# Kernel optimization log

Hardware: AMD Instinct MI355X
Metric: run time of the kernel (lower is better)

Reference implementation:

```python
import jax, jax.numpy as jnp
import numpy as np

TOP_K = 2
NUM_EXPERTS = 64
SEQ, BS, HS = 2048, 4, 4096
TOKENS = SEQ * BS  # tokens_per_batch
TOL = 1e-4
EPS = 1e-8


def sinkhorn(temp_cost):
    # temp_cost: (T, E) float32 logits. Mirrors SinkhornRouter.sinkhorn exactly.
    cost = jnp.exp(temp_cost)
    n0, n1 = cost.shape
    # initial d0 (overwritten inside loop in torch too, kept for fidelity of carry dtype/shape)
    d0 = (TOKENS / NUM_EXPERTS) * jnp.sum(jnp.exp(2.0 * temp_cost), axis=1)
    d1 = jnp.ones((n1,), dtype=cost.dtype)
    err0 = jnp.asarray(1e9, dtype=cost.dtype)

    def cond(carry):
        _, _, err = carry
        return err > TOL

    def body(carry):
        d0, d1, _ = carry  # d1 here plays the role of d1_old
        d0_new = (1.0 / n0) / (jnp.sum(d1 * cost, axis=1) + EPS)          # (T,)
        d1_new = (1.0 / n1) / (jnp.sum(d0_new[:, None] * cost, axis=0) + EPS)  # (E,)
        err = jnp.mean(jnp.abs(d1 - d1_new))
        return (d0_new, d1_new, err)

    d0, d1, _ = jax.lax.while_loop(cond, body, (d0, d1, err0))
    return d1 * cost * d0[:, None]


def setup_inputs() -> dict:
    key = jax.random.key(0)
    kx, kw = jax.random.split(key)
    x = jax.random.normal(kx, (SEQ, BS, HS), dtype=jnp.float32)
    W = jax.random.normal(kw, (NUM_EXPERTS, HS), dtype=jnp.float32) * 0.02
    return {"x": x, "W": W}


def reference(x, W):
    # router logits: (T, E)
    logits = jnp.reshape(x, (-1, x.shape[-1])) @ W.T
    # Sinkhorn normalization is done in fp32 under no_grad in torch -> stop_gradient
    norm_logits = sinkhorn(jax.lax.stop_gradient(logits).astype(jnp.float32))
    _, indices = jax.lax.top_k(norm_logits, TOP_K)  # (T, top_k) int32
    # top_k > 1 -> softmax activation (fp32, cast back)
    probs = jax.nn.softmax(logits.astype(jnp.float32), axis=-1).astype(logits.dtype)
    scores = jnp.take_along_axis(probs, indices, axis=1)  # (T, top_k)
    return scores, indices
```

## Files before the change

kernel.cpp:

```cpp
#include <hip/hip_runtime.h>
#include <hip/hip_cooperative_groups.h>
#include <math.h>

namespace cg = cooperative_groups;

namespace {
constexpr int kTokens = 8192;
constexpr int kHS = 4096;
constexpr float kTol = 1e-4f;
constexpr float kEps = 1e-8f;
constexpr int kMaxIters = 1000;
constexpr int kSinkBlocks = 64;
constexpr size_t kTagFloats = 128;
constexpr size_t kGdataFloats = 2 * 64 * 64;
constexpr size_t kLogitsOff = kTagFloats + kGdataFloats;
constexpr size_t kLogitsFloats = (size_t)kTokens * 64;
constexpr size_t kWtpFloats = (size_t)(kHS / 4) * 64 * 4;
}

__device__ __forceinline__ float wave_sum(float v) {
#pragma unroll
  for (int o = 32; o; o >>= 1) v += __shfl_xor(v, o, 64);
  return v;
}

typedef __attribute__((ext_vector_type(8))) short bf16x8;
typedef __attribute__((ext_vector_type(4))) float f32x4;

__device__ __forceinline__ unsigned short f2bf(float x) {
  unsigned u = __builtin_bit_cast(unsigned, x);
  u += 0x7fffu + ((u >> 16) & 1u);
  return (unsigned short)(u >> 16);
}

__device__ __forceinline__ void split8(const float* p, bf16x8& hi, bf16x8& lo) {
  const float4 a = *(const float4*)p;
  const float4 b = *(const float4*)(p + 4);
  const float v[8] = {a.x, a.y, a.z, a.w, b.x, b.y, b.z, b.w};
#pragma unroll
  for (int j = 0; j < 8; ++j) {
    const unsigned short h = f2bf(v[j]);
    const float hf = __builtin_bit_cast(float, (unsigned)h << 16);
    hi[j] = (short)h;
    lo[j] = (short)f2bf(v[j] - hf);
  }
}

__global__ void __launch_bounds__(512, 2)
k_logits(const float* __restrict__ X, const float* __restrict__ W,
         float* __restrict__ logits) {
  const int tid = threadIdx.x;
  const int lane = tid & 63;
  const int wid = tid >> 6;
  const int t0 = blockIdx.x * 32;
  const int r = lane & 15;
  const int g = lane >> 4;

  const float* xp = X + (size_t)(t0 + r) * kHS + wid * 512 + g * 8;
  const float* wp = W + (size_t)r * kHS + wid * 512 + g * 8;

  f32x4 acc[2][4];
#pragma unroll
  for (int m = 0; m < 2; ++m)
#pragma unroll
    for (int n = 0; n < 4; ++n) acc[m][n] = (f32x4){0.f, 0.f, 0.f, 0.f};

#pragma unroll 2
  for (int ks = 0; ks < 16; ++ks) {
    const int ko = ks * 32;
    bf16x8 ah[2], al[2], bh[4], bl[4];
#pragma unroll
    for (int m = 0; m < 2; ++m)
      split8(xp + (size_t)(16 * m) * kHS + ko, ah[m], al[m]);
#pragma unroll
    for (int n = 0; n < 4; ++n)
      split8(wp + (size_t)(16 * n) * kHS + ko, bh[n], bl[n]);
#pragma unroll
    for (int m = 0; m < 2; ++m)
#pragma unroll
      for (int n = 0; n < 4; ++n) {
        acc[m][n] = __builtin_amdgcn_mfma_f32_16x16x32_bf16(ah[m], bh[n],
                                                            acc[m][n], 0, 0, 0);
        acc[m][n] = __builtin_amdgcn_mfma_f32_16x16x32_bf16(al[m], bh[n],
                                                            acc[m][n], 0, 0, 0);
        acc[m][n] = __builtin_amdgcn_mfma_f32_16x16x32_bf16(ah[m], bl[n],
                                                            acc[m][n], 0, 0, 0);
      }
  }

  __shared__ __align__(16) float red[8][32][68];
#pragma unroll
  for (int m = 0; m < 2; ++m)
#pragma unroll
    for (int n = 0; n < 4; ++n)
#pragma unroll
      for (int q = 0; q < 4; ++q)
        red[wid][m * 16 + g * 4 + q][n * 16 + r] = acc[m][n][q];
  __syncthreads();

  const int t = tid >> 4;
  const int e4 = (tid & 15) * 4;
  float4 s = *(const float4*)&red[0][t][e4];
#pragma unroll
  for (int w = 1; w < 8; ++w) {
    const float4 p = *(const float4*)&red[w][t][e4];
    s.x += p.x; s.y += p.y; s.z += p.z; s.w += p.w;
  }
  *(float4*)(logits + (size_t)(t0 + t) * 64 + e4) = s;
}

__global__ void __launch_bounds__(1024, 1)
k_sinkhorn(const float* __restrict__ logits, float* __restrict__ out,
           unsigned* __restrict__ tags, float* __restrict__ gdata) {
  const int tid = threadIdx.x;
  const int lane = tid & 63;
  const int wid = __builtin_amdgcn_readfirstlane(tid >> 6);
  const int blk = blockIdx.x;
  __shared__ float lds[1024];

  const int t0 = blk * 128 + wid * 8;
  float lg[8], cst[8];
#pragma unroll
  for (int t = 0; t < 8; ++t) {
    const float a = logits[(size_t)(t0 + t) * 64 + lane];
    lg[t] = a;
    cst[t] = expf(a);
  }

  float d1 = 1.0f;
  float d0v[8];
  int buf = 0;
  for (int it = 0; it < kMaxIters; ++it) {
    float p = 0.0f;
#pragma unroll
    for (int t = 0; t < 8; ++t) {
      const float s = wave_sum(d1 * cst[t]);
      const float d0t = (1.0f / 8192.0f) / (s + kEps);
      d0v[t] = d0t;
      p = fmaf(d0t, cst[t], p);
    }
    __syncthreads();
    lds[wid * 64 + lane] = p;
    __syncthreads();
    const unsigned want = (unsigned)(it + 1);
    if (wid == 0) {
      float bp = 0.0f;
#pragma unroll
      for (int w = 0; w < 16; ++w) bp += lds[w * 64 + lane];
      __hip_atomic_store(&gdata[((size_t)buf * 64 + blk) * 64 + lane], bp,
                         __ATOMIC_RELAXED, __HIP_MEMORY_SCOPE_AGENT);
      __threadfence();
      if (lane == 0)
        __hip_atomic_store(&tags[buf * 64 + blk], want, __ATOMIC_RELEASE,
                           __HIP_MEMORY_SCOPE_AGENT);
      while (__hip_atomic_load(&tags[buf * 64 + lane], __ATOMIC_ACQUIRE,
                               __HIP_MEMORY_SCOPE_AGENT) != want) {
        __builtin_amdgcn_s_sleep(1);
      }
    }
    __syncthreads();
    float s2 = 0.0f;
#pragma unroll
    for (int i = 0; i < 4; ++i)
      s2 += __hip_atomic_load(
          &gdata[((size_t)buf * 64 + wid * 4 + i) * 64 + lane],
          __ATOMIC_RELAXED, __HIP_MEMORY_SCOPE_AGENT);
    lds[wid * 64 + lane] = s2;
    __syncthreads();
    float colsum = 0.0f;
#pragma unroll
    for (int w = 0; w < 16; ++w) colsum += lds[w * 64 + lane];
    const float d1n = (1.0f / 64.0f) / (colsum + kEps);
    const float err = wave_sum(fabsf(d1 - d1n)) * (1.0f / 64.0f);
    d1 = d1n;
    buf ^= 1;
    if (err <= kTol) break;
  }

#pragma unroll
  for (int t = 0; t < 8; ++t) {
    const float lgv = lg[t];
    float m = lgv;
#pragma unroll
    for (int o = 32; o; o >>= 1) m = fmaxf(m, __shfl_xor(m, o, 64));
    const float ex = expf(lgv - m);
    const float den = wave_sum(ex);
    const float prob = ex / den;

    const float v = (d1 * cst[t]) * d0v[t];
    float v1 = v;
    int i1 = lane;
#pragma unroll
    for (int o = 32; o; o >>= 1) {
      const float ov = __shfl_xor(v1, o, 64);
      const int oi = __shfl_xor(i1, o, 64);
      if (ov > v1 || (ov == v1 && oi < i1)) { v1 = ov; i1 = oi; }
    }
    float v2 = (lane == i1) ? -INFINITY : v;
    int i2 = lane;
#pragma unroll
    for (int o = 32; o; o >>= 1) {
      const float ov = __shfl_xor(v2, o, 64);
      const int oi = __shfl_xor(i2, o, 64);
      if (ov > v2 || (ov == v2 && oi < i2)) { v2 = ov; i2 = oi; }
    }
    const float p1 = __shfl(prob, i1, 64);
    const float p2 = __shfl(prob, i2, 64);
    if (lane == 0) {
      const int row = t0 + t;
      out[row * 2 + 0] = p1;
      out[row * 2 + 1] = p2;
      out[2 * kTokens + row * 2 + 0] = (float)i1;
      out[2 * kTokens + row * 2 + 1] = (float)i2;
    }
  }
}

__global__ void __launch_bounds__(256, 1)
sinkhorn_router(const float* __restrict__ X, const float* __restrict__ W,
                float* __restrict__ out, float* __restrict__ ws) {
  cg::grid_group grid = cg::this_grid();
  const int tid = threadIdx.x;
  const int lane = tid & 63;
  const int wid = __builtin_amdgcn_readfirstlane(tid >> 6);
  const int blk = blockIdx.x;

  float4* wtp = reinterpret_cast<float4*>(ws);
  float* gpart = ws + kWtpFloats;
  __shared__ float lds[256];

  {
    const int j = blk * 256 + tid;
    const int e = j & 63;
    const int k4 = j >> 6;
    wtp[j] = *reinterpret_cast<const float4*>(W + (size_t)e * kHS + 4 * (size_t)k4);
  }
  grid.sync();

  const int t0 = blk * 32 + wid * 8;
  const float* xb = X + (size_t)t0 * kHS;
  float lg[8];
#pragma unroll
  for (int t = 0; t < 8; ++t) lg[t] = 0.0f;

#pragma unroll 2
  for (int k4 = 0; k4 < kHS / 4; ++k4) {
    const float4 w = wtp[k4 * 64 + lane];
#pragma unroll
    for (int t = 0; t < 8; ++t) {
      const float* xr = xb + (size_t)t * kHS + 4 * (size_t)k4;
      float a = lg[t];
      a = fmaf(xr[0], w.x, a);
      a = fmaf(xr[1], w.y, a);
      a = fmaf(xr[2], w.z, a);
      a = fmaf(xr[3], w.w, a);
      lg[t] = a;
    }
  }

  float cst[8];
#pragma unroll
  for (int t = 0; t < 8; ++t) cst[t] = expf(lg[t]);

  float d1 = 1.0f;
  float d0v[8];
  int buf = 0;
  for (int it = 0; it < kMaxIters; ++it) {
    float p = 0.0f;
#pragma unroll
    for (int t = 0; t < 8; ++t) {
      const float s = wave_sum(d1 * cst[t]);
      const float d0t = (1.0f / 8192.0f) / (s + kEps);
      d0v[t] = d0t;
      p = fmaf(d0t, cst[t], p);
    }
    __syncthreads();
    lds[wid * 64 + lane] = p;
    __syncthreads();
    if (wid == 0) {
      const float bp =
          lds[lane] + lds[64 + lane] + lds[128 + lane] + lds[192 + lane];
      gpart[buf * (256 * 64) + blk * 64 + lane] = bp;
    }
    grid.sync();
    const float* gp = gpart + buf * (256 * 64);
    float s = 0.0f;
#pragma unroll 8
    for (int b = 0; b < 64; ++b) s += gp[(wid * 64 + b) * 64 + lane];
    lds[wid * 64 + lane] = s;
    __syncthreads();
    const float colsum =
        lds[lane] + lds[64 + lane] + lds[128 + lane] + lds[192 + lane];
    const float d1n = (1.0f / 64.0f) / (colsum + kEps);
    const float err = wave_sum(fabsf(d1 - d1n)) * (1.0f / 64.0f);
    d1 = d1n;
    buf ^= 1;
    if (err <= kTol) break;
  }

#pragma unroll
  for (int t = 0; t < 8; ++t) {
    const float lgv = lg[t];
    float m = lgv;
#pragma unroll
    for (int o = 32; o; o >>= 1) m = fmaxf(m, __shfl_xor(m, o, 64));
    const float ex = expf(lgv - m);
    const float den = wave_sum(ex);
    const float prob = ex / den;

    const float v = (d1 * cst[t]) * d0v[t];
    float v1 = v;
    int i1 = lane;
#pragma unroll
    for (int o = 32; o; o >>= 1) {
      const float ov = __shfl_xor(v1, o, 64);
      const int oi = __shfl_xor(i1, o, 64);
      if (ov > v1 || (ov == v1 && oi < i1)) { v1 = ov; i1 = oi; }
    }
    float v2 = (lane == i1) ? -INFINITY : v;
    int i2 = lane;
#pragma unroll
    for (int o = 32; o; o >>= 1) {
      const float ov = __shfl_xor(v2, o, 64);
      const int oi = __shfl_xor(i2, o, 64);
      if (ov > v2 || (ov == v2 && oi < i2)) { v2 = ov; i2 = oi; }
    }
    const float p1 = __shfl(prob, i1, 64);
    const float p2 = __shfl(prob, i2, 64);
    if (lane == 0) {
      const int row = t0 + t;
      out[row * 2 + 0] = p1;
      out[row * 2 + 1] = p2;
      out[2 * kTokens + row * 2 + 0] = (float)i1;
      out[2 * kTokens + row * 2 + 1] = (float)i2;
    }
  }
}

extern "C" void kernel_launch(void* const* d_in, const int* in_sizes, int n_in,
                              void* d_out, int out_size, void* d_ws,
                              size_t ws_size, hipStream_t stream) {
  const float* X = (const float*)d_in[0];
  const float* W = (const float*)d_in[1];
  float* out = (float*)d_out;
  float* ws = (float*)d_ws;

  const size_t need = (kLogitsOff + kLogitsFloats) * sizeof(float);
  if (ws_size < need) {
    void* args[] = {(void*)&X, (void*)&W, (void*)&out, (void*)&ws};
    hipLaunchCooperativeKernel((const void*)sinkhorn_router, dim3(256),
                               dim3(256), args, 0, stream);
    return;
  }

  unsigned* tags = reinterpret_cast<unsigned*>(ws);
  float* gdata = ws + kTagFloats;
  float* logits = ws + kLogitsOff;

  hipLaunchKernelGGL(k_logits, dim3(kTokens / 32), dim3(512), 0, stream, X, W,
                     logits);
  hipLaunchKernelGGL(k_sinkhorn, dim3(kSinkBlocks), dim3(1024), 0, stream,
                     logits, out, tags, gdata);
}
```

Before: 269.0 us.

## Pre-split W into bf16 hi/lo MFMA fragments and shrink logits tile

Adds a small pre-pass kernel that converts W once into bf16 hi/lo pairs stored in MFMA fragment order, so the logits kernel no longer re-splits W in every block. The logits kernel now handles 16 tokens per block instead of 32, with one M tile per wave and higher occupancy bounds. X loads are batched four k-steps at a time to hide latency. This adds an extra launch and more workspace, and halves reuse of W per block.

```diff
diff --git a/kernel.cpp b/kernel.cpp
--- a/kernel.cpp
+++ b/kernel.cpp
@@ -15,6 +15,10 @@
 constexpr size_t kGdataFloats = 2 * 64 * 64;
 constexpr size_t kLogitsOff = kTagFloats + kGdataFloats;
 constexpr size_t kLogitsFloats = (size_t)kTokens * 64;
+constexpr size_t kWhiOff = kLogitsOff + kLogitsFloats;
+constexpr size_t kWFragFloats = (size_t)(kHS / 32) * 4 * 64 * 4;
+constexpr size_t kWloOff = kWhiOff + kWFragFloats;
+constexpr size_t kWsNeedFloats = kWloOff + kWFragFloats;
 constexpr size_t kWtpFloats = (size_t)(kHS / 4) * 64 * 4;
 }
 
@@ -33,9 +37,8 @@
   return (unsigned short)(u >> 16);
 }
 
-__device__ __forceinline__ void split8(const float* p, bf16x8& hi, bf16x8& lo) {
-  const float4 a = *(const float4*)p;
-  const float4 b = *(const float4*)(p + 4);
+__device__ __forceinline__ void split8r(const float4 a, const float4 b,
+                                        bf16x8& hi, bf16x8& lo) {
   const float v[8] = {a.x, a.y, a.z, a.w, b.x, b.y, b.z, b.w};
 #pragma unroll
   for (int j = 0; j < 8; ++j) {
@@ -46,67 +49,92 @@
   }
 }
 
-__global__ void __launch_bounds__(512, 2)
-k_logits(const float* __restrict__ X, const float* __restrict__ W,
-         float* __restrict__ logits) {
+__device__ __forceinline__ void split8(const float* p, bf16x8& hi, bf16x8& lo) {
+  split8r(*(const float4*)p, *(const float4*)(p + 4), hi, lo);
+}
+
+__global__ void __launch_bounds__(256)
+k_wsplit(const float* __restrict__ W, bf16x8* __restrict__ whi,
+         bf16x8* __restrict__ wlo) {
+  const int idx = blockIdx.x * 256 + threadIdx.x;
+  const int lane = idx & 63;
+  const int n = (idx >> 6) & 3;
+  const int kk = idx >> 8;
+  const int e = 16 * n + (lane & 15);
+  const int k = kk * 32 + ((lane >> 4) << 3);
+  bf16x8 hi, lo;
+  split8(W + (size_t)e * kHS + k, hi, lo);
+  whi[idx] = hi;
+  wlo[idx] = lo;
+}
+
+__global__ void __launch_bounds__(512, 4)
+k_logits(const float* __restrict__ X, const bf16x8* __restrict__ whi,
+         const bf16x8* __restrict__ wlo, float* __restrict__ logits) {
   const int tid = threadIdx.x;
   const int lane = tid & 63;
   const int wid = tid >> 6;
-  const int t0 = blockIdx.x * 32;
+  const int t0 = blockIdx.x * 16;
   const int r = lane & 15;
   const int g = lane >> 4;
 
   const float* xp = X + (size_t)(t0 + r) * kHS + wid * 512 + g * 8;
-  const float* wp = W + (size_t)r * kHS + wid * 512 + g * 8;
-
-  f32x4 acc[2][4];
-#pragma unroll
-  for (int m = 0; m < 2; ++m)
-#pragma unroll
-    for (int n = 0; n < 4; ++n) acc[m][n] = (f32x4){0.f, 0.f, 0.f, 0.f};
-
-#pragma unroll 2
-  for (int ks = 0; ks < 16; ++ks) {
-    const int ko = ks * 32;
-    bf16x8 ah[2], al[2], bh[4], bl[4];
-#pragma unroll
-    for (int m = 0; m < 2; ++m)
-      split8(xp + (size_t)(16 * m) * kHS + ko, ah[m], al[m]);
-#pragma unroll
-    for (int n = 0; n < 4; ++n)
-      split8(wp + (size_t)(16 * n) * kHS + ko, bh[n], bl[n]);
-#pragma unroll
-    for (int m = 0; m < 2; ++m)
+  const bf16x8* bh_base = whi + (size_t)wid * 16 * 4 * 64 + lane;
+  const bf16x8* bl_base = wlo + (size_t)wid * 16 * 4 * 64 + lane;
+
+  f32x4 acc[4];
+#pragma unroll
+  for (int n = 0; n < 4; ++n) acc[n] = (f32x4){0.f, 0.f, 0.f, 0.f};
+
+#pragma unroll
+  for (int c = 0; c < 4; ++c) {
+    float4 xa[4][2];
+#pragma unroll
+    for (int i = 0; i < 4; ++i) {
+      const float* p = xp + (size_t)(c * 4 + i) * 32;
+      xa[i][0] = *(const float4*)p;
+      xa[i][1] = *(const float4*)(p + 4);
+    }
+#pragma unroll
+    for (int i = 0; i < 4; ++i) {
+      const int ks = c * 4 + i;
+      bf16x8 bh[4], bl[4];
 #pragma unroll
       for (int n = 0; n < 4; ++n) {
-        acc[m][n] = __builtin_amdgcn_mfma_f32_16x16x32_bf16(ah[m], bh[n],
-                                                            acc[m][n], 0, 0, 0);
-        acc[m][n] = __builtin_amdgcn_mfma_f32_16x16x32_bf16(al[m], bh[n],
-                                                            acc[m][n], 0, 0, 0);
-        acc[m][n] = __builtin_amdgcn_mfma_f32_16x16x32_bf16(ah[m], bl[n],
-                                                            acc[m][n], 0, 0, 0);
+        bh[n] = bh_base[(ks * 4 + n) * 64];
+        bl[n] = bl_base[(ks * 4 + n) * 64];
       }
-  }
-
-  __shared__ __align__(16) float red[8][32][68];
-#pragma unroll
-  for (int m = 0; m < 2; ++m)
-#pragma unroll
-    for (int n = 0; n < 4; ++n)
-#pragma unroll
-      for (int q = 0; q < 4; ++q)
-        red[wid][m * 16 + g * 4 + q][n * 16 + r] = acc[m][n][q];
+      bf16x8 ah, al;
+      split8r(xa[i][0], xa[i][1], ah, al);
+#pragma unroll
+      for (int n = 0; n < 4; ++n) {
+        acc[n] = __builtin_amdgcn_mfma_f32_16x16x32_bf16(ah, bh[n], acc[n],
+                                                         0, 0, 0);
+        acc[n] = __builtin_amdgcn_mfma_f32_16x16x32_bf16(al, bh[n], acc[n],
+                                                         0, 0, 0);
+        acc[n] = __builtin_amdgcn_mfma_f32_16x16x32_bf16(ah, bl[n], acc[n],
+                                                         0, 0, 0);
+      }
+    }
+  }
+
+  __shared__ __align__(16) float red[8][16][68];
+#pragma unroll
+  for (int n = 0; n < 4; ++n)
+#pragma unroll
+    for (int q = 0; q < 4; ++q)
+      red[wid][g * 4 + q][n * 16 + r] = acc[n][q];
   __syncthreads();
 
-  const int t = tid >> 4;
-  const int e4 = (tid & 15) * 4;
-  float4 s = *(const float4*)&red[0][t][e4];
-#pragma unroll
-  for (int w = 1; w < 8; ++w) {
-    const float4 p = *(const float4*)&red[w][t][e4];
-    s.x += p.x; s.y += p.y; s.z += p.z; s.w += p.w;
-  }
-  *(float4*)(logits + (size_t)(t0 + t) * 64 + e4) = s;
+  const int t = tid >> 5;
+  const int e2 = (tid & 31) * 2;
+  float2 s = make_float2(0.f, 0.f);
+#pragma unroll
+  for (int w = 0; w < 8; ++w) {
+    s.x += red[w][t][e2];
+    s.y += red[w][t][e2 + 1];
+  }
+  *(float2*)(logits + (size_t)(t0 + t) * 64 + e2) = s;
 }
 
 __global__ void __launch_bounds__(1024, 1)
@@ -345,7 +373,7 @@
   float* out = (float*)d_out;
   float* ws = (float*)d_ws;
 
-  const size_t need = (kLogitsOff + kLogitsFloats) * sizeof(float);
+  const size_t need = kWsNeedFloats * sizeof(float);
   if (ws_size < need) {
     void* args[] = {(void*)&X, (void*)&W, (void*)&out, (void*)&ws};
     hipLaunchCooperativeKernel((const void*)sinkhorn_router, dim3(256),
@@ -356,9 +384,13 @@
   unsigned* tags = reinterpret_cast<unsigned*>(ws);
   float* gdata = ws + kTagFloats;
   float* logits = ws + kLogitsOff;
-
-  hipLaunchKernelGGL(k_logits, dim3(kTokens / 32), dim3(512), 0, stream, X, W,
-                     logits);
+  bf16x8* whi = reinterpret_cast<bf16x8*>(ws + kWhiOff);
+  bf16x8* wlo = reinterpret_cast<bf16x8*>(ws + kWloOff);
+
+  hipLaunchKernelGGL(k_wsplit, dim3((kHS / 32) * 4 * 64 / 256), dim3(256), 0,
+                     stream, W, whi, wlo);
+  hipLaunchKernelGGL(k_logits, dim3(kTokens / 16), dim3(512), 0, stream, X,
+                     whi, wlo, logits);
   hipLaunchKernelGGL(k_sinkhorn, dim3(kSinkBlocks), dim3(1024), 0, stream,
                      logits, out, tags, gdata);
 }
```

New measurement: 248.4 us. -7.7%, faster.
